# Kernel tuning notes

Measured on AMD Instinct MI355X. Metric: run time of the kernel, lower is better.

The kernel has to match this reference:

```python
import jax, jax.numpy as jnp
import numpy as np

N_NODES = 50000
N_EDGES = 800000
D_IN = 128
D_OUT = 128


def _seg_mean(values, seg_ids, num_segments):
    # values: [E, D] gathered messages; seg_ids: [E] destination ids
    s = jax.ops.segment_sum(values, seg_ids, num_segments=num_segments)
    deg = jax.ops.segment_sum(jnp.ones((values.shape[0],), values.dtype), seg_ids,
                              num_segments=num_segments)
    # DGL mean aggregation yields 0 for zero in-degree nodes
    return jnp.where(deg[:, None] > 0, s / jnp.maximum(deg, 1.0)[:, None], 0.0)


def setup_inputs() -> dict:
    key = jax.random.key(0)
    k1, k2, k3, k4, k5 = jax.random.split(key, 5)
    feat = jax.random.normal(k1, (N_NODES, D_IN), dtype=jnp.float32)
    src = jax.random.randint(k2, (N_EDGES,), 0, N_NODES, dtype=jnp.int32)
    dst = jax.random.randint(k3, (N_EDGES,), 0, N_NODES, dtype=jnp.int32)
    W = jax.random.normal(k4, (D_OUT, 3 * D_IN), dtype=jnp.float32) * (1.0 / np.sqrt(3 * D_IN))
    b = jax.random.normal(k5, (D_OUT,), dtype=jnp.float32) * 0.01
    return {"feat": feat, "src": src, "dst": dst, "W": W, "b": b}


def reference(feat, src, dst, W, b):
    n = feat.shape[0]
    # forward direction: message from src -> dst, mean over in-neighbors
    fwd_neigh = _seg_mean(feat[src], dst, n)          # [N, D]
    # backward direction: graph.reverse() swaps src/dst
    bwd_neigh = _seg_mean(feat[dst], src, n)          # [N, D]
    h = jnp.concatenate((feat, fwd_neigh, bwd_neigh), axis=1)  # [N, 3D]
    return h @ W.T + b
```

## Files before the change

kernel.cpp:

```cpp
#include <hip/hip_runtime.h>

#define DIM 128
#define CAP 64
#define CHUNK 2048

typedef __attribute__((ext_vector_type(8))) short bf16x8;
typedef __attribute__((ext_vector_type(4))) float f32x4;
typedef __attribute__((ext_vector_type(2))) float f32x2;

__device__ __forceinline__ unsigned short f2b(float f) {
  unsigned int u = __float_as_uint(f);
  return (unsigned short)((u + 0x7FFFu + ((u >> 16) & 1u)) >> 16);
}
__device__ __forceinline__ float blo(unsigned int v) { return __uint_as_float(v << 16); }
__device__ __forceinline__ float bhi(unsigned int v) { return __uint_as_float(v & 0xFFFF0000u); }

__global__ void k_prep(const float* __restrict__ feat, const float* __restrict__ W,
                       unsigned short* __restrict__ featb, unsigned short* __restrict__ Wb,
                       int N) {
  int i = blockIdx.x * blockDim.x + threadIdx.x;
  int ftotal = N * (DIM / 4);
  if (i < ftotal) {
    float4 v = ((const float4*)feat)[i];
    ushort4 o; o.x = f2b(v.x); o.y = f2b(v.y); o.z = f2b(v.z); o.w = f2b(v.w);
    ((ushort4*)featb)[i] = o;
  }
  const int wtotal = DIM * 3 * DIM / 4;
  if (i < wtotal) {
    float4 v = ((const float4*)W)[i];
    ushort4 o; o.x = f2b(v.x); o.y = f2b(v.y); o.z = f2b(v.z); o.w = f2b(v.w);
    ((ushort4*)Wb)[i] = o;
  }
}

__global__ __launch_bounds__(256) void k_gemmT(
    const unsigned short* __restrict__ featb, const unsigned short* __restrict__ Wb,
    const float* __restrict__ bias, unsigned short* __restrict__ g1b,
    unsigned char* __restrict__ g2f8, unsigned char* __restrict__ g3f8, int N) {
  const int wave = threadIdx.x >> 6, lane = threadIdx.x & 63;
  const int lr = lane & 15, lk = lane >> 4;
  const int nc = blockIdx.y;
  const int W0 = blockIdx.x * 4 + wave;
  const int TW = gridDim.x * 4;

  bf16x8 bf[4][4];
  #pragma unroll
  for (int kc = 0; kc < 4; ++kc)
    #pragma unroll
    for (int nf = 0; nf < 4; ++nf) {
      int n = nc * 64 + nf * 16 + lr;
      bf[kc][nf] = *(const bf16x8*)(Wb + (size_t)(n & 127) * 384 + (n >> 7) * 128
                                       + kc * 32 + lk * 8);
    }
  float bv[4];
  if (nc < 2) {
    #pragma unroll
    for (int nf = 0; nf < 4; ++nf) bv[nf] = bias[nc * 64 + nf * 16 + lr];
  }

  const int T = N >> 4;
  for (int t = W0; t < T; t += TW) {
    const int m0 = t * 16;
    bf16x8 a[4];
    #pragma unroll
    for (int kc = 0; kc < 4; ++kc)
      a[kc] = *(const bf16x8*)(featb + (size_t)(m0 + lr) * DIM + kc * 32 + lk * 8);
    f32x4 acc[4];
    #pragma unroll
    for (int nf = 0; nf < 4; ++nf) acc[nf] = (f32x4){0.f, 0.f, 0.f, 0.f};
    #pragma unroll
    for (int kc = 0; kc < 4; ++kc)
      #pragma unroll
      for (int nf = 0; nf < 4; ++nf)
        acc[nf] = __builtin_amdgcn_mfma_f32_16x16x32_bf16(a[kc], bf[kc][nf], acc[nf], 0, 0, 0);
    if (nc < 2) {
      #pragma unroll
      for (int nf = 0; nf < 4; ++nf)
        #pragma unroll
        for (int j = 0; j < 4; ++j)
          g1b[(size_t)(m0 + lk * 4 + j) * DIM + nc * 64 + nf * 16 + lr] =
              f2b(acc[nf][j] + bv[nf]);
    } else {
      unsigned char* gp = (nc < 4) ? g2f8 : g3f8;
      const int c0 = (nc & 1) * 64;
      #pragma unroll
      for (int nf = 0; nf < 4; ++nf)
        #pragma unroll
        for (int j = 0; j < 4; ++j) {
          unsigned int p8 = __builtin_amdgcn_cvt_pk_fp8_f32(acc[nf][j], acc[nf][j], 0, 0);
          gp[(size_t)(m0 + lk * 4 + j) * DIM + c0 + nf * 16 + lr] = (unsigned char)p8;
        }
    }
  }
}

__global__ __launch_bounds__(256) void k_bin(const int* __restrict__ src,
                                             const int* __restrict__ dst,
                                             unsigned int* __restrict__ scrF,
                                             unsigned int* __restrict__ scrB,
                                             int* __restrict__ offsF,
                                             int* __restrict__ offsB, int E) {
  __shared__ int fc[256], bc[256], fo[256], bo[256], sa[256], sb2[256];
  __shared__ unsigned int linf[CHUNK], linb[CHUNK];
  const int t = threadIdx.x;
  const int base = blockIdx.x * CHUNK;
  const int n = min(CHUNK, E - base);
  fc[t] = 0; bc[t] = 0;
  __syncthreads();
  int fbk[8], fsl[8], bsl[8], bbk[8];
  unsigned int fvv[8], bvv[8];
  #pragma unroll
  for (int j = 0; j < 8; ++j) {
    int e = base + j * 256 + t;
    fbk[j] = -1;
    if (e < E) {
      int s = src[e], d = dst[e];
      fbk[j] = d >> 8; fvv[j] = ((unsigned int)(d & 255) << 16) | (unsigned int)s;
      bbk[j] = s >> 8; bvv[j] = ((unsigned int)(s & 255) << 16) | (unsigned int)d;
      fsl[j] = atomicAdd(&fc[fbk[j]], 1);
      bsl[j] = atomicAdd(&bc[bbk[j]], 1);
    }
  }
  __syncthreads();
  sa[t] = fc[t]; sb2[t] = bc[t];
  __syncthreads();
  #pragma unroll
  for (int s = 1; s < 256; s <<= 1) {
    int va = sa[t] + ((t >= s) ? sa[t - s] : 0);
    int vb = sb2[t] + ((t >= s) ? sb2[t - s] : 0);
    __syncthreads();
    sa[t] = va; sb2[t] = vb;
    __syncthreads();
  }
  fo[t] = sa[t] - fc[t];
  bo[t] = sb2[t] - bc[t];
  __syncthreads();
  #pragma unroll
  for (int j = 0; j < 8; ++j) {
    if (fbk[j] >= 0) {
      linf[fo[fbk[j]] + fsl[j]] = fvv[j];
      linb[bo[bbk[j]] + bsl[j]] = bvv[j];
    }
  }
  offsF[blockIdx.x * 256 + t] = fo[t];
  offsB[blockIdx.x * 256 + t] = bo[t];
  __syncthreads();
  for (int k = t; k < n; k += 256) {
    scrF[base + k] = linf[k];
    scrB[base + k] = linb[k];
  }
}

__global__ __launch_bounds__(512) void k_csr(const unsigned int* __restrict__ scrF,
                                             const unsigned int* __restrict__ scrB,
                                             const int* __restrict__ offsF,
                                             const int* __restrict__ offsB,
                                             unsigned short* __restrict__ fnbr,
                                             unsigned short* __restrict__ bnbr,
                                             int* __restrict__ degF, int* __restrict__ degB,
                                             int N, int E, int nblk) {
  __shared__ int ncnt[256];
  __shared__ unsigned short nbuf[256][CAP];
  const int b = blockIdx.x;
  const int dir = blockIdx.y;
  const unsigned int* scr = dir ? scrB : scrF;
  const int* offs = dir ? offsB : offsF;
  const int t = threadIdx.x;
  if (t < 256) ncnt[t] = 0;
  __syncthreads();
  for (int i = t; i < nblk; i += 512) {
    int o = offs[i * 256 + b];
    int n = min(CHUNK, E - i * CHUNK);
    int nxt = (b < 255) ? offs[i * 256 + b + 1] : n;
    int cb = i * CHUNK;
    for (int k = o; k < nxt; ++k) {
      unsigned int v = scr[cb + k];
      int node8 = v >> 16;
      int slot = atomicAdd(&ncnt[node8], 1);
      if (slot < CAP) nbuf[node8][slot] = (unsigned short)(v & 0xFFFFu);
    }
  }
  __syncthreads();
  const int node0 = b * 256;
  const int nvalid = min(256, N - node0);
  if (nvalid <= 0) return;
  unsigned short* outp = (dir ? bnbr : fnbr) + (size_t)node0 * CAP;
  for (int idx = t; idx < nvalid * CAP; idx += 512)
    outp[idx] = nbuf[idx >> 6][idx & 63];
  int* deg = dir ? degB : degF;
  for (int u = t; u < nvalid; u += 512) deg[node0 + u] = ncnt[u];
}

__global__ void k_aggregate(const unsigned char* __restrict__ g2f8,
                            const unsigned char* __restrict__ g3f8,
                            const unsigned short* __restrict__ g1b,
                            const int* __restrict__ degF, const int* __restrict__ degB,
                            const unsigned short* __restrict__ fnbr,
                            const unsigned short* __restrict__ bnbr,
                            float* __restrict__ out, int N) {
  int node = blockIdx.x * (blockDim.x >> 6) + (threadIdx.x >> 6);
  if (node >= N) return;
  const int lane = threadIdx.x & 63;
  const int qg = lane >> 4;
  const int sub = lane & 15;

  const int degf = degF[node], degb = degB[node];
  const int capf = min(degf, CAP), capb = min(degb, CAP);
  const int fid = fnbr[(size_t)node * CAP + lane];
  const int bid = bnbr[(size_t)node * CAP + lane];

  const uint2* gf = (const uint2*)g2f8;
  const uint2* gb = (const uint2*)g3f8;
  float fa0=0,fa1=0,fa2=0,fa3=0,fa4=0,fa5=0,fa6=0,fa7=0;
  float ba0=0,ba1=0,ba2=0,ba3=0,ba4=0,ba5=0,ba6=0,ba7=0;
  const int gmax = (max(capf, capb) + 3) >> 2;
  #pragma unroll 4
  for (int g = 0; g < gmax; ++g) {
    int k = 4 * g + qg;
    int rf = __shfl(fid, k);
    int rb = __shfl(bid, k);
    if (k < capf) {
      uint2 v = gf[(size_t)rf * 16 + sub];
      f32x2 p0 = __builtin_amdgcn_cvt_pk_f32_fp8(v.x, 0);
      f32x2 p1 = __builtin_amdgcn_cvt_pk_f32_fp8(v.x, 1);
      f32x2 p2 = __builtin_amdgcn_cvt_pk_f32_fp8(v.y, 0);
      f32x2 p3 = __builtin_amdgcn_cvt_pk_f32_fp8(v.y, 1);
      fa0 += p0[0]; fa1 += p0[1]; fa2 += p1[0]; fa3 += p1[1];
      fa4 += p2[0]; fa5 += p2[1]; fa6 += p3[0]; fa7 += p3[1];
    }
    if (k < capb) {
      uint2 v = gb[(size_t)rb * 16 + sub];
      f32x2 p0 = __builtin_amdgcn_cvt_pk_f32_fp8(v.x, 0);
      f32x2 p1 = __builtin_amdgcn_cvt_pk_f32_fp8(v.x, 1);
      f32x2 p2 = __builtin_amdgcn_cvt_pk_f32_fp8(v.y, 0);
      f32x2 p3 = __builtin_amdgcn_cvt_pk_f32_fp8(v.y, 1);
      ba0 += p0[0]; ba1 += p0[1]; ba2 += p1[0]; ba3 += p1[1];
      ba4 += p2[0]; ba5 += p2[1]; ba6 += p3[0]; ba7 += p3[1];
    }
  }
  fa0 += __shfl_xor(fa0, 16); fa0 += __shfl_xor(fa0, 32);
  fa1 += __shfl_xor(fa1, 16); fa1 += __shfl_xor(fa1, 32);
  fa2 += __shfl_xor(fa2, 16); fa2 += __shfl_xor(fa2, 32);
  fa3 += __shfl_xor(fa3, 16); fa3 += __shfl_xor(fa3, 32);
  fa4 += __shfl_xor(fa4, 16); fa4 += __shfl_xor(fa4, 32);
  fa5 += __shfl_xor(fa5, 16); fa5 += __shfl_xor(fa5, 32);
  fa6 += __shfl_xor(fa6, 16); fa6 += __shfl_xor(fa6, 32);
  fa7 += __shfl_xor(fa7, 16); fa7 += __shfl_xor(fa7, 32);
  ba0 += __shfl_xor(ba0, 16); ba0 += __shfl_xor(ba0, 32);
  ba1 += __shfl_xor(ba1, 16); ba1 += __shfl_xor(ba1, 32);
  ba2 += __shfl_xor(ba2, 16); ba2 += __shfl_xor(ba2, 32);
  ba3 += __shfl_xor(ba3, 16); ba3 += __shfl_xor(ba3, 32);
  ba4 += __shfl_xor(ba4, 16); ba4 += __shfl_xor(ba4, 32);
  ba5 += __shfl_xor(ba5, 16); ba5 += __shfl_xor(ba5, 32);
  ba6 += __shfl_xor(ba6, 16); ba6 += __shfl_xor(ba6, 32);
  ba7 += __shfl_xor(ba7, 16); ba7 += __shfl_xor(ba7, 32);

  if (lane < 16) {
    const float sf = (degf > 0) ? 1.0f / (float)degf : 0.0f;
    const float sb = (degb > 0) ? 1.0f / (float)degb : 0.0f;
    uint4 g1v = ((const uint4*)g1b)[(size_t)node * 16 + lane];
    float4 u, v;
    u.x = blo(g1v.x) + fa0 * sf + ba0 * sb;
    u.y = bhi(g1v.x) + fa1 * sf + ba1 * sb;
    u.z = blo(g1v.y) + fa2 * sf + ba2 * sb;
    u.w = bhi(g1v.y) + fa3 * sf + ba3 * sb;
    v.x = blo(g1v.z) + fa4 * sf + ba4 * sb;
    v.y = bhi(g1v.z) + fa5 * sf + ba5 * sb;
    v.z = blo(g1v.w) + fa6 * sf + ba6 * sb;
    v.w = bhi(g1v.w) + fa7 * sf + ba7 * sb;
    float* op = out + (size_t)node * DIM + lane * 8;
    *(float4*)op = u; *(float4*)(op + 4) = v;
  }
}

extern "C" void kernel_launch(void* const* d_in, const int* in_sizes, int n_in,
                              void* d_out, int out_size, void* d_ws, size_t ws_size,
                              hipStream_t stream) {
  (void)n_in; (void)out_size; (void)ws_size;
  const float* feat = (const float*)d_in[0];
  const int*   src  = (const int*)d_in[1];
  const int*   dst  = (const int*)d_in[2];
  const float* W    = (const float*)d_in[3];
  const float* bias = (const float*)d_in[4];
  float* out = (float*)d_out;
  const int N = in_sizes[0] / DIM;
  const int E = in_sizes[1];
  const int nblk = (E + CHUNK - 1) / CHUNK;
  const int nbkt = (N + 255) / 256;

  char* ws = (char*)d_ws;
  size_t off = 0;
  auto take = [&](size_t bytes) -> void* {
    off = (off + 255) & ~(size_t)255;
    void* p = ws + off;
    off += bytes;
    return p;
  };
  unsigned int* scrF = (unsigned int*)take((size_t)nblk * CHUNK * 4);
  unsigned int* scrB = (unsigned int*)take((size_t)nblk * CHUNK * 4);
  int* offsF = (int*)take((size_t)nblk * 256 * 4);
  int* offsB = (int*)take((size_t)nblk * 256 * 4);
  unsigned short* fnbr = (unsigned short*)take((size_t)N * CAP * 2);
  unsigned short* bnbr = (unsigned short*)take((size_t)N * CAP * 2);
  int* degF = (int*)take((size_t)N * 4);
  int* degB = (int*)take((size_t)N * 4);
  unsigned short* featb = (unsigned short*)take((size_t)N * DIM * 2);
  unsigned short* Wb    = (unsigned short*)take((size_t)DIM * 3 * DIM * 2);
  unsigned short* g1b   = (unsigned short*)take((size_t)N * DIM * 2);
  unsigned char*  g2f8  = (unsigned char*)take((size_t)N * DIM);
  unsigned char*  g3f8  = (unsigned char*)take((size_t)N * DIM);

  int prep_threads = N * 32;
  k_prep<<<(prep_threads + 255) / 256, 256, 0, stream>>>(feat, W, featb, Wb, N);
  k_gemmT<<<dim3(128, 6), 256, 0, stream>>>(featb, Wb, bias, g1b, g2f8, g3f8, N);
  k_bin<<<nblk, 256, 0, stream>>>(src, dst, scrF, scrB, offsF, offsB, E);
  k_csr<<<dim3(nbkt, 2), 512, 0, stream>>>(scrF, scrB, offsF, offsB,
                                           fnbr, bnbr, degF, degB, N, E, nblk);
  k_aggregate<<<(N + 3) / 4, 256, 0, stream>>>(g2f8, g3f8, g1b, degF, degB,
                                               fnbr, bnbr, out, N);
}
```

Before: 104.0 us.

## Fuse prep with binning and CSR build with aggregation, prefetch GEMM A tiles

Merges the bf16 conversion kernel with the edge binning kernel into one launch, selected by block index, and fuses the CSR bucket build with the neighbor aggregation so neighbor lists and degrees stay in shared memory instead of going through global memory. The GEMM loop now loads the next A tile before computing the current one. The fused CSR/aggregate kernel runs only about 196 blocks of 512 threads, each aggregating 256 nodes, so much less parallelism is available for the gather-heavy aggregation phase, and it uses about 64KB of shared memory per block.

```diff
diff --git a/kernel.cpp b/kernel.cpp
--- a/kernel.cpp
+++ b/kernel.cpp
@@ -15,21 +15,78 @@
 __device__ __forceinline__ float blo(unsigned int v) { return __uint_as_float(v << 16); }
 __device__ __forceinline__ float bhi(unsigned int v) { return __uint_as_float(v & 0xFFFF0000u); }
 
-__global__ void k_prep(const float* __restrict__ feat, const float* __restrict__ W,
-                       unsigned short* __restrict__ featb, unsigned short* __restrict__ Wb,
-                       int N) {
-  int i = blockIdx.x * blockDim.x + threadIdx.x;
-  int ftotal = N * (DIM / 4);
-  if (i < ftotal) {
-    float4 v = ((const float4*)feat)[i];
-    ushort4 o; o.x = f2b(v.x); o.y = f2b(v.y); o.z = f2b(v.z); o.w = f2b(v.w);
-    ((ushort4*)featb)[i] = o;
-  }
-  const int wtotal = DIM * 3 * DIM / 4;
-  if (i < wtotal) {
-    float4 v = ((const float4*)W)[i];
-    ushort4 o; o.x = f2b(v.x); o.y = f2b(v.y); o.z = f2b(v.z); o.w = f2b(v.w);
-    ((ushort4*)Wb)[i] = o;
+__global__ __launch_bounds__(256) void k_prepbin(
+    const float* __restrict__ feat, const float* __restrict__ W,
+    const int* __restrict__ src, const int* __restrict__ dst,
+    unsigned short* __restrict__ featb, unsigned short* __restrict__ Wb,
+    unsigned int* __restrict__ scrF, unsigned int* __restrict__ scrB,
+    int* __restrict__ offsF, int* __restrict__ offsB, int N, int E, int nblk) {
+  __shared__ int fc[256], bc[256], fo[256], bo[256], sa[256], sb2[256];
+  __shared__ unsigned int linf[CHUNK], linb[CHUNK];
+  const int t = threadIdx.x;
+
+  if (blockIdx.x >= nblk) {
+    int i = (blockIdx.x - nblk) * 256 + t;
+    int ftotal = N * (DIM / 4);
+    if (i < ftotal) {
+      float4 v = ((const float4*)feat)[i];
+      ushort4 o; o.x = f2b(v.x); o.y = f2b(v.y); o.z = f2b(v.z); o.w = f2b(v.w);
+      ((ushort4*)featb)[i] = o;
+    }
+    const int wtotal = DIM * 3 * DIM / 4;
+    if (i < wtotal) {
+      float4 v = ((const float4*)W)[i];
+      ushort4 o; o.x = f2b(v.x); o.y = f2b(v.y); o.z = f2b(v.z); o.w = f2b(v.w);
+      ((ushort4*)Wb)[i] = o;
+    }
+    return;
+  }
+
+  const int base = blockIdx.x * CHUNK;
+  const int n = min(CHUNK, E - base);
+  fc[t] = 0; bc[t] = 0;
+  __syncthreads();
+  int fbk[8], fsl[8], bsl[8], bbk[8];
+  unsigned int fvv[8], bvv[8];
+  #pragma unroll
+  for (int j = 0; j < 8; ++j) {
+    int e = base + j * 256 + t;
+    fbk[j] = -1;
+    if (e < E) {
+      int s = src[e], d = dst[e];
+      fbk[j] = d >> 8; fvv[j] = ((unsigned int)(d & 255) << 16) | (unsigned int)s;
+      bbk[j] = s >> 8; bvv[j] = ((unsigned int)(s & 255) << 16) | (unsigned int)d;
+      fsl[j] = atomicAdd(&fc[fbk[j]], 1);
+      bsl[j] = atomicAdd(&bc[bbk[j]], 1);
+    }
+  }
+  __syncthreads();
+  sa[t] = fc[t]; sb2[t] = bc[t];
+  __syncthreads();
+  #pragma unroll
+  for (int s = 1; s < 256; s <<= 1) {
+    int va = sa[t] + ((t >= s) ? sa[t - s] : 0);
+    int vb = sb2[t] + ((t >= s) ? sb2[t - s] : 0);
+    __syncthreads();
+    sa[t] = va; sb2[t] = vb;
+    __syncthreads();
+  }
+  fo[t] = sa[t] - fc[t];
+  bo[t] = sb2[t] - bc[t];
+  __syncthreads();
+  #pragma unroll
+  for (int j = 0; j < 8; ++j) {
+    if (fbk[j] >= 0) {
+      linf[fo[fbk[j]] + fsl[j]] = fvv[j];
+      linb[bo[bbk[j]] + bsl[j]] = bvv[j];
+    }
+  }
+  offsF[blockIdx.x * 256 + t] = fo[t];
+  offsB[blockIdx.x * 256 + t] = bo[t];
+  __syncthreads();
+  for (int k = t; k < n; k += 256) {
+    scrF[base + k] = linf[k];
+    scrB[base + k] = linb[k];
   }
 }
 
@@ -59,12 +116,22 @@
   }
 
   const int T = N >> 4;
-  for (int t = W0; t < T; t += TW) {
+  int t = W0;
+  bf16x8 a[4];
+  if (t < T) {
+    #pragma unroll
+    for (int kc = 0; kc < 4; ++kc)
+      a[kc] = *(const bf16x8*)(featb + (size_t)(t * 16 + lr) * DIM + kc * 32 + lk * 8);
+  }
+  while (t < T) {
+    const int tn = t + TW;
+    bf16x8 an[4];
+    if (tn < T) {
+      #pragma unroll
+      for (int kc = 0; kc < 4; ++kc)
+        an[kc] = *(const bf16x8*)(featb + (size_t)(tn * 16 + lr) * DIM + kc * 32 + lk * 8);
+    }
     const int m0 = t * 16;
-    bf16x8 a[4];
-    #pragma unroll
-    for (int kc = 0; kc < 4; ++kc)
-      a[kc] = *(const bf16x8*)(featb + (size_t)(m0 + lr) * DIM + kc * 32 + lk * 8);
     f32x4 acc[4];
     #pragma unroll
     for (int nf = 0; nf < 4; ++nf) acc[nf] = (f32x4){0.f, 0.f, 0.f, 0.f};
@@ -91,185 +158,118 @@
           gp[(size_t)(m0 + lk * 4 + j) * DIM + c0 + nf * 16 + lr] = (unsigned char)p8;
         }
     }
-  }
-}
-
-__global__ __launch_bounds__(256) void k_bin(const int* __restrict__ src,
-                                             const int* __restrict__ dst,
-                                             unsigned int* __restrict__ scrF,
-                                             unsigned int* __restrict__ scrB,
-                                             int* __restrict__ offsF,
-                                             int* __restrict__ offsB, int E) {
-  __shared__ int fc[256], bc[256], fo[256], bo[256], sa[256], sb2[256];
-  __shared__ unsigned int linf[CHUNK], linb[CHUNK];
+    #pragma unroll
+    for (int kc = 0; kc < 4; ++kc) a[kc] = an[kc];
+    t = tn;
+  }
+}
+
+__global__ __launch_bounds__(512) void k_csragg(
+    const unsigned int* __restrict__ scrF, const unsigned int* __restrict__ scrB,
+    const int* __restrict__ offsF, const int* __restrict__ offsB,
+    const unsigned char* __restrict__ g2f8, const unsigned char* __restrict__ g3f8,
+    const unsigned short* __restrict__ g1b, float* __restrict__ out,
+    int N, int E, int nblk) {
+  __shared__ int ncF[256], ncB[256];
+  __shared__ unsigned short nbF[256][CAP], nbB[256][CAP];
+  const int b = blockIdx.x;
   const int t = threadIdx.x;
-  const int base = blockIdx.x * CHUNK;
-  const int n = min(CHUNK, E - base);
-  fc[t] = 0; bc[t] = 0;
-  __syncthreads();
-  int fbk[8], fsl[8], bsl[8], bbk[8];
-  unsigned int fvv[8], bvv[8];
-  #pragma unroll
-  for (int j = 0; j < 8; ++j) {
-    int e = base + j * 256 + t;
-    fbk[j] = -1;
-    if (e < E) {
-      int s = src[e], d = dst[e];
-      fbk[j] = d >> 8; fvv[j] = ((unsigned int)(d & 255) << 16) | (unsigned int)s;
-      bbk[j] = s >> 8; bvv[j] = ((unsigned int)(s & 255) << 16) | (unsigned int)d;
-      fsl[j] = atomicAdd(&fc[fbk[j]], 1);
-      bsl[j] = atomicAdd(&bc[bbk[j]], 1);
-    }
-  }
-  __syncthreads();
-  sa[t] = fc[t]; sb2[t] = bc[t];
-  __syncthreads();
-  #pragma unroll
-  for (int s = 1; s < 256; s <<= 1) {
-    int va = sa[t] + ((t >= s) ? sa[t - s] : 0);
-    int vb = sb2[t] + ((t >= s) ? sb2[t - s] : 0);
-    __syncthreads();
-    sa[t] = va; sb2[t] = vb;
-    __syncthreads();
-  }
-  fo[t] = sa[t] - fc[t];
-  bo[t] = sb2[t] - bc[t];
-  __syncthreads();
-  #pragma unroll
-  for (int j = 0; j < 8; ++j) {
-    if (fbk[j] >= 0) {
-      linf[fo[fbk[j]] + fsl[j]] = fvv[j];
-      linb[bo[bbk[j]] + bsl[j]] = bvv[j];
-    }
-  }
-  offsF[blockIdx.x * 256 + t] = fo[t];
-  offsB[blockIdx.x * 256 + t] = bo[t];
-  __syncthreads();
-  for (int k = t; k < n; k += 256) {
-    scrF[base + k] = linf[k];
-    scrB[base + k] = linb[k];
-  }
-}
-
-__global__ __launch_bounds__(512) void k_csr(const unsigned int* __restrict__ scrF,
-                                             const unsigned int* __restrict__ scrB,
-                                             const int* __restrict__ offsF,
-                                             const int* __restrict__ offsB,
-                                             unsigned short* __restrict__ fnbr,
-                                             unsigned short* __restrict__ bnbr,
-                                             int* __restrict__ degF, int* __restrict__ degB,
-                                             int N, int E, int nblk) {
-  __shared__ int ncnt[256];
-  __shared__ unsigned short nbuf[256][CAP];
-  const int b = blockIdx.x;
-  const int dir = blockIdx.y;
-  const unsigned int* scr = dir ? scrB : scrF;
-  const int* offs = dir ? offsB : offsF;
-  const int t = threadIdx.x;
-  if (t < 256) ncnt[t] = 0;
+  if (t < 256) { ncF[t] = 0; ncB[t] = 0; }
   __syncthreads();
   for (int i = t; i < nblk; i += 512) {
-    int o = offs[i * 256 + b];
-    int n = min(CHUNK, E - i * CHUNK);
-    int nxt = (b < 255) ? offs[i * 256 + b + 1] : n;
-    int cb = i * CHUNK;
-    for (int k = o; k < nxt; ++k) {
-      unsigned int v = scr[cb + k];
-      int node8 = v >> 16;
-      int slot = atomicAdd(&ncnt[node8], 1);
-      if (slot < CAP) nbuf[node8][slot] = (unsigned short)(v & 0xFFFFu);
-    }
-  }
-  __syncthreads();
-  const int node0 = b * 256;
-  const int nvalid = min(256, N - node0);
-  if (nvalid <= 0) return;
-  unsigned short* outp = (dir ? bnbr : fnbr) + (size_t)node0 * CAP;
-  for (int idx = t; idx < nvalid * CAP; idx += 512)
-    outp[idx] = nbuf[idx >> 6][idx & 63];
-  int* deg = dir ? degB : degF;
-  for (int u = t; u < nvalid; u += 512) deg[node0 + u] = ncnt[u];
-}
-
-__global__ void k_aggregate(const unsigned char* __restrict__ g2f8,
-                            const unsigned char* __restrict__ g3f8,
-                            const unsigned short* __restrict__ g1b,
-                            const int* __restrict__ degF, const int* __restrict__ degB,
-                            const unsigned short* __restrict__ fnbr,
-                            const unsigned short* __restrict__ bnbr,
-                            float* __restrict__ out, int N) {
-  int node = blockIdx.x * (blockDim.x >> 6) + (threadIdx.x >> 6);
-  if (node >= N) return;
-  const int lane = threadIdx.x & 63;
+    const int cb = i * CHUNK;
+    const int n = min(CHUNK, E - cb);
+    int o = offsF[i * 256 + b];
+    int nx = (b < 255) ? offsF[i * 256 + b + 1] : n;
+    for (int k = o; k < nx; ++k) {
+      unsigned int v = scrF[cb + k];
+      int n8 = v >> 16;
+      int sl = atomicAdd(&ncF[n8], 1);
+      if (sl < CAP) nbF[n8][sl] = (unsigned short)(v & 0xFFFFu);
+    }
+    o = offsB[i * 256 + b];
+    nx = (b < 255) ? offsB[i * 256 + b + 1] : n;
+    for (int k = o; k < nx; ++k) {
+      unsigned int v = scrB[cb + k];
+      int n8 = v >> 16;
+      int sl = atomicAdd(&ncB[n8], 1);
+      if (sl < CAP) nbB[n8][sl] = (unsigned short)(v & 0xFFFFu);
+    }
+  }
+  __syncthreads();
+
+  const int wv = t >> 6, lane = t & 63;
   const int qg = lane >> 4;
   const int sub = lane & 15;
-
-  const int degf = degF[node], degb = degB[node];
-  const int capf = min(degf, CAP), capb = min(degb, CAP);
-  const int fid = fnbr[(size_t)node * CAP + lane];
-  const int bid = bnbr[(size_t)node * CAP + lane];
-
   const uint2* gf = (const uint2*)g2f8;
   const uint2* gb = (const uint2*)g3f8;
-  float fa0=0,fa1=0,fa2=0,fa3=0,fa4=0,fa5=0,fa6=0,fa7=0;
-  float ba0=0,ba1=0,ba2=0,ba3=0,ba4=0,ba5=0,ba6=0,ba7=0;
-  const int gmax = (max(capf, capb) + 3) >> 2;
-  #pragma unroll 4
-  for (int g = 0; g < gmax; ++g) {
-    int k = 4 * g + qg;
-    int rf = __shfl(fid, k);
-    int rb = __shfl(bid, k);
-    if (k < capf) {
-      uint2 v = gf[(size_t)rf * 16 + sub];
-      f32x2 p0 = __builtin_amdgcn_cvt_pk_f32_fp8(v.x, 0);
-      f32x2 p1 = __builtin_amdgcn_cvt_pk_f32_fp8(v.x, 1);
-      f32x2 p2 = __builtin_amdgcn_cvt_pk_f32_fp8(v.y, 0);
-      f32x2 p3 = __builtin_amdgcn_cvt_pk_f32_fp8(v.y, 1);
-      fa0 += p0[0]; fa1 += p0[1]; fa2 += p1[0]; fa3 += p1[1];
-      fa4 += p2[0]; fa5 += p2[1]; fa6 += p3[0]; fa7 += p3[1];
-    }
-    if (k < capb) {
-      uint2 v = gb[(size_t)rb * 16 + sub];
-      f32x2 p0 = __builtin_amdgcn_cvt_pk_f32_fp8(v.x, 0);
-      f32x2 p1 = __builtin_amdgcn_cvt_pk_f32_fp8(v.x, 1);
-      f32x2 p2 = __builtin_amdgcn_cvt_pk_f32_fp8(v.y, 0);
-      f32x2 p3 = __builtin_amdgcn_cvt_pk_f32_fp8(v.y, 1);
-      ba0 += p0[0]; ba1 += p0[1]; ba2 += p1[0]; ba3 += p1[1];
-      ba4 += p2[0]; ba5 += p2[1]; ba6 += p3[0]; ba7 += p3[1];
-    }
-  }
-  fa0 += __shfl_xor(fa0, 16); fa0 += __shfl_xor(fa0, 32);
-  fa1 += __shfl_xor(fa1, 16); fa1 += __shfl_xor(fa1, 32);
-  fa2 += __shfl_xor(fa2, 16); fa2 += __shfl_xor(fa2, 32);
-  fa3 += __shfl_xor(fa3, 16); fa3 += __shfl_xor(fa3, 32);
-  fa4 += __shfl_xor(fa4, 16); fa4 += __shfl_xor(fa4, 32);
-  fa5 += __shfl_xor(fa5, 16); fa5 += __shfl_xor(fa5, 32);
-  fa6 += __shfl_xor(fa6, 16); fa6 += __shfl_xor(fa6, 32);
-  fa7 += __shfl_xor(fa7, 16); fa7 += __shfl_xor(fa7, 32);
-  ba0 += __shfl_xor(ba0, 16); ba0 += __shfl_xor(ba0, 32);
-  ba1 += __shfl_xor(ba1, 16); ba1 += __shfl_xor(ba1, 32);
-  ba2 += __shfl_xor(ba2, 16); ba2 += __shfl_xor(ba2, 32);
-  ba3 += __shfl_xor(ba3, 16); ba3 += __shfl_xor(ba3, 32);
-  ba4 += __shfl_xor(ba4, 16); ba4 += __shfl_xor(ba4, 32);
-  ba5 += __shfl_xor(ba5, 16); ba5 += __shfl_xor(ba5, 32);
-  ba6 += __shfl_xor(ba6, 16); ba6 += __shfl_xor(ba6, 32);
-  ba7 += __shfl_xor(ba7, 16); ba7 += __shfl_xor(ba7, 32);
-
-  if (lane < 16) {
-    const float sf = (degf > 0) ? 1.0f / (float)degf : 0.0f;
-    const float sb = (degb > 0) ? 1.0f / (float)degb : 0.0f;
-    uint4 g1v = ((const uint4*)g1b)[(size_t)node * 16 + lane];
-    float4 u, v;
-    u.x = blo(g1v.x) + fa0 * sf + ba0 * sb;
-    u.y = bhi(g1v.x) + fa1 * sf + ba1 * sb;
-    u.z = blo(g1v.y) + fa2 * sf + ba2 * sb;
-    u.w = bhi(g1v.y) + fa3 * sf + ba3 * sb;
-    v.x = blo(g1v.z) + fa4 * sf + ba4 * sb;
-    v.y = bhi(g1v.z) + fa5 * sf + ba5 * sb;
-    v.z = blo(g1v.w) + fa6 * sf + ba6 * sb;
-    v.w = bhi(g1v.w) + fa7 * sf + ba7 * sb;
-    float* op = out + (size_t)node * DIM + lane * 8;
-    *(float4*)op = u; *(float4*)(op + 4) = v;
+
+  for (int j = 0; j < 32; ++j) {
+    const int n8 = wv * 32 + j;
+    const int node = b * 256 + n8;
+    if (node >= N) break;
+    const int degf = ncF[n8], degb = ncB[n8];
+    const int capf = min(degf, CAP), capb = min(degb, CAP);
+    f32x2 f01 = {0.f, 0.f}, f23 = {0.f, 0.f}, f45 = {0.f, 0.f}, f67 = {0.f, 0.f};
+    f32x2 b01 = {0.f, 0.f}, b23 = {0.f, 0.f}, b45 = {0.f, 0.f}, b67 = {0.f, 0.f};
+    const int gmax = (max(capf, capb) + 3) >> 2;
+    #pragma unroll 4
+    for (int g = 0; g < gmax; ++g) {
+      int k = 4 * g + qg;
+      if (k < capf) {
+        int rf = nbF[n8][k];
+        uint2 v = gf[(size_t)rf * 16 + sub];
+        f01 += __builtin_amdgcn_cvt_pk_f32_fp8(v.x, 0);
+        f23 += __builtin_amdgcn_cvt_pk_f32_fp8(v.x, 1);
+        f45 += __builtin_amdgcn_cvt_pk_f32_fp8(v.y, 0);
+        f67 += __builtin_amdgcn_cvt_pk_f32_fp8(v.y, 1);
+      }
+      if (k < capb) {
+        int rb = nbB[n8][k];
+        uint2 v = gb[(size_t)rb * 16 + sub];
+        b01 += __builtin_amdgcn_cvt_pk_f32_fp8(v.x, 0);
+        b23 += __builtin_amdgcn_cvt_pk_f32_fp8(v.x, 1);
+        b45 += __builtin_amdgcn_cvt_pk_f32_fp8(v.y, 0);
+        b67 += __builtin_amdgcn_cvt_pk_f32_fp8(v.y, 1);
+      }
+    }
+    float fa0 = f01[0], fa1 = f01[1], fa2 = f23[0], fa3 = f23[1];
+    float fa4 = f45[0], fa5 = f45[1], fa6 = f67[0], fa7 = f67[1];
+    float ba0 = b01[0], ba1 = b01[1], ba2 = b23[0], ba3 = b23[1];
+    float ba4 = b45[0], ba5 = b45[1], ba6 = b67[0], ba7 = b67[1];
+    fa0 += __shfl_xor(fa0, 16); fa0 += __shfl_xor(fa0, 32);
+    fa1 += __shfl_xor(fa1, 16); fa1 += __shfl_xor(fa1, 32);
+    fa2 += __shfl_xor(fa2, 16); fa2 += __shfl_xor(fa2, 32);
+    fa3 += __shfl_xor(fa3, 16); fa3 += __shfl_xor(fa3, 32);
+    fa4 += __shfl_xor(fa4, 16); fa4 += __shfl_xor(fa4, 32);
+    fa5 += __shfl_xor(fa5, 16); fa5 += __shfl_xor(fa5, 32);
+    fa6 += __shfl_xor(fa6, 16); fa6 += __shfl_xor(fa6, 32);
+    fa7 += __shfl_xor(fa7, 16); fa7 += __shfl_xor(fa7, 32);
+    ba0 += __shfl_xor(ba0, 16); ba0 += __shfl_xor(ba0, 32);
+    ba1 += __shfl_xor(ba1, 16); ba1 += __shfl_xor(ba1, 32);
+    ba2 += __shfl_xor(ba2, 16); ba2 += __shfl_xor(ba2, 32);
+    ba3 += __shfl_xor(ba3, 16); ba3 += __shfl_xor(ba3, 32);
+    ba4 += __shfl_xor(ba4, 16); ba4 += __shfl_xor(ba4, 32);
+    ba5 += __shfl_xor(ba5, 16); ba5 += __shfl_xor(ba5, 32);
+    ba6 += __shfl_xor(ba6, 16); ba6 += __shfl_xor(ba6, 32);
+    ba7 += __shfl_xor(ba7, 16); ba7 += __shfl_xor(ba7, 32);
+
+    if (lane < 16) {
+      const float sf = (degf > 0) ? 1.0f / (float)degf : 0.0f;
+      const float sb = (degb > 0) ? 1.0f / (float)degb : 0.0f;
+      uint4 g1v = ((const uint4*)g1b)[(size_t)node * 16 + lane];
+      float4 u, v;
+      u.x = blo(g1v.x) + fa0 * sf + ba0 * sb;
+      u.y = bhi(g1v.x) + fa1 * sf + ba1 * sb;
+      u.z = blo(g1v.y) + fa2 * sf + ba2 * sb;
+      u.w = bhi(g1v.y) + fa3 * sf + ba3 * sb;
+      v.x = blo(g1v.z) + fa4 * sf + ba4 * sb;
+      v.y = bhi(g1v.z) + fa5 * sf + ba5 * sb;
+      v.z = blo(g1v.w) + fa6 * sf + ba6 * sb;
+      v.w = bhi(g1v.w) + fa7 * sf + ba7 * sb;
+      float* op = out + (size_t)node * DIM + lane * 8;
+      *(float4*)op = u; *(float4*)(op + 4) = v;
+    }
   }
 }
 
@@ -300,22 +300,16 @@
   unsigned int* scrB = (unsigned int*)take((size_t)nblk * CHUNK * 4);
   int* offsF = (int*)take((size_t)nblk * 256 * 4);
   int* offsB = (int*)take((size_t)nblk * 256 * 4);
-  unsigned short* fnbr = (unsigned short*)take((size_t)N * CAP * 2);
-  unsigned short* bnbr = (unsigned short*)take((size_t)N * CAP * 2);
-  int* degF = (int*)take((size_t)N * 4);
-  int* degB = (int*)take((size_t)N * 4);
   unsigned short* featb = (unsigned short*)take((size_t)N * DIM * 2);
   unsigned short* Wb    = (unsigned short*)take((size_t)DIM * 3 * DIM * 2);
   unsigned short* g1b   = (unsigned short*)take((size_t)N * DIM * 2);
   unsigned char*  g2f8  = (unsigned char*)take((size_t)N * DIM);
   unsigned char*  g3f8  = (unsigned char*)take((size_t)N * DIM);
 
-  int prep_threads = N * 32;
-  k_prep<<<(prep_threads + 255) / 256, 256, 0, stream>>>(feat, W, featb, Wb, N);
+  const int prep_blocks = (N * 32 + 255) / 256;
+  k_prepbin<<<nblk + prep_blocks, 256, 0, stream>>>(
+      feat, W, src, dst, featb, Wb, scrF, scrB, offsF, offsB, N, E, nblk);
   k_gemmT<<<dim3(128, 6), 256, 0, stream>>>(featb, Wb, bias, g1b, g2f8, g3f8, N);
-  k_bin<<<nblk, 256, 0, stream>>>(src, dst, scrF, scrB, offsF, offsB, E);
-  k_csr<<<dim3(nbkt, 2), 512, 0, stream>>>(scrF, scrB, offsF, offsB,
-                                           fnbr, bnbr, degF, degB, N, E, nblk);
-  k_aggregate<<<(N + 3) / 4, 256, 0, stream>>>(g2f8, g3f8, g1b, degF, degB,
-                                               fnbr, bnbr, out, N);
-}
+  k_csragg<<<nbkt, 512, 0, stream>>>(scrF, scrB, offsF, offsB,
+                                     g2f8, g3f8, g1b, out, N, E, nblk);
+}
```

Measured after the change: 190.4 us. 1.83x slower.

## Merge independent kernels into combined launches, prefetch GEMM tiles, pack fp8 accumulation

Applied to the files above, without the earlier changes.

The prep and bin kernels are merged into one launch, with blocks partitioned by index. The CSR-build and GEMM kernels are merged the same way, so independent work runs concurrently and launch gaps shrink from five kernels to three. The GEMM loop now software-prefetches the next A tile, using 512-thread blocks with 8 waves. The aggregate loop accumulates into packed f32x2 vectors with a deeper unroll. The merged kernels carry the larger LDS footprint onto all blocks, which may reduce occupancy for the prep and GEMM blocks.

```diff
diff --git a/kernel.cpp b/kernel.cpp
--- a/kernel.cpp
+++ b/kernel.cpp
@@ -15,33 +15,131 @@
 __device__ __forceinline__ float blo(unsigned int v) { return __uint_as_float(v << 16); }
 __device__ __forceinline__ float bhi(unsigned int v) { return __uint_as_float(v & 0xFFFF0000u); }
 
-__global__ void k_prep(const float* __restrict__ feat, const float* __restrict__ W,
-                       unsigned short* __restrict__ featb, unsigned short* __restrict__ Wb,
-                       int N) {
-  int i = blockIdx.x * blockDim.x + threadIdx.x;
-  int ftotal = N * (DIM / 4);
-  if (i < ftotal) {
-    float4 v = ((const float4*)feat)[i];
-    ushort4 o; o.x = f2b(v.x); o.y = f2b(v.y); o.z = f2b(v.z); o.w = f2b(v.w);
-    ((ushort4*)featb)[i] = o;
-  }
-  const int wtotal = DIM * 3 * DIM / 4;
-  if (i < wtotal) {
-    float4 v = ((const float4*)W)[i];
-    ushort4 o; o.x = f2b(v.x); o.y = f2b(v.y); o.z = f2b(v.z); o.w = f2b(v.w);
-    ((ushort4*)Wb)[i] = o;
-  }
-}
-
-__global__ __launch_bounds__(256) void k_gemmT(
+__global__ __launch_bounds__(256) void k_prepbin(
+    const float* __restrict__ feat, const float* __restrict__ W,
+    const int* __restrict__ src, const int* __restrict__ dst,
+    unsigned short* __restrict__ featb, unsigned short* __restrict__ Wb,
+    unsigned int* __restrict__ scrF, unsigned int* __restrict__ scrB,
+    int* __restrict__ offsF, int* __restrict__ offsB, int N, int E, int nblk) {
+  __shared__ int fc[256], bc[256], fo[256], bo[256], sa[256], sb2[256];
+  __shared__ unsigned int linf[CHUNK], linb[CHUNK];
+  const int t = threadIdx.x;
+
+  if (blockIdx.x >= nblk) {
+    int i = (blockIdx.x - nblk) * 256 + t;
+    int ftotal = N * (DIM / 4);
+    if (i < ftotal) {
+      float4 v = ((const float4*)feat)[i];
+      ushort4 o; o.x = f2b(v.x); o.y = f2b(v.y); o.z = f2b(v.z); o.w = f2b(v.w);
+      ((ushort4*)featb)[i] = o;
+    }
+    const int wtotal = DIM * 3 * DIM / 4;
+    if (i < wtotal) {
+      float4 v = ((const float4*)W)[i];
+      ushort4 o; o.x = f2b(v.x); o.y = f2b(v.y); o.z = f2b(v.z); o.w = f2b(v.w);
+      ((ushort4*)Wb)[i] = o;
+    }
+    return;
+  }
+
+  const int base = blockIdx.x * CHUNK;
+  const int n = min(CHUNK, E - base);
+  fc[t] = 0; bc[t] = 0;
+  __syncthreads();
+  int fbk[8], fsl[8], bsl[8], bbk[8];
+  unsigned int fvv[8], bvv[8];
+  #pragma unroll
+  for (int j = 0; j < 8; ++j) {
+    int e = base + j * 256 + t;
+    fbk[j] = -1;
+    if (e < E) {
+      int s = src[e], d = dst[e];
+      fbk[j] = d >> 8; fvv[j] = ((unsigned int)(d & 255) << 16) | (unsigned int)s;
+      bbk[j] = s >> 8; bvv[j] = ((unsigned int)(s & 255) << 16) | (unsigned int)d;
+      fsl[j] = atomicAdd(&fc[fbk[j]], 1);
+      bsl[j] = atomicAdd(&bc[bbk[j]], 1);
+    }
+  }
+  __syncthreads();
+  sa[t] = fc[t]; sb2[t] = bc[t];
+  __syncthreads();
+  #pragma unroll
+  for (int s = 1; s < 256; s <<= 1) {
+    int va = sa[t] + ((t >= s) ? sa[t - s] : 0);
+    int vb = sb2[t] + ((t >= s) ? sb2[t - s] : 0);
+    __syncthreads();
+    sa[t] = va; sb2[t] = vb;
+    __syncthreads();
+  }
+  fo[t] = sa[t] - fc[t];
+  bo[t] = sb2[t] - bc[t];
+  __syncthreads();
+  #pragma unroll
+  for (int j = 0; j < 8; ++j) {
+    if (fbk[j] >= 0) {
+      linf[fo[fbk[j]] + fsl[j]] = fvv[j];
+      linb[bo[bbk[j]] + bsl[j]] = bvv[j];
+    }
+  }
+  offsF[blockIdx.x * 256 + t] = fo[t];
+  offsB[blockIdx.x * 256 + t] = bo[t];
+  __syncthreads();
+  for (int k = t; k < n; k += 256) {
+    scrF[base + k] = linf[k];
+    scrB[base + k] = linb[k];
+  }
+}
+
+__global__ __launch_bounds__(512) void k_gemmcsr(
     const unsigned short* __restrict__ featb, const unsigned short* __restrict__ Wb,
     const float* __restrict__ bias, unsigned short* __restrict__ g1b,
-    unsigned char* __restrict__ g2f8, unsigned char* __restrict__ g3f8, int N) {
-  const int wave = threadIdx.x >> 6, lane = threadIdx.x & 63;
+    unsigned char* __restrict__ g2f8, unsigned char* __restrict__ g3f8,
+    const unsigned int* __restrict__ scrF, const unsigned int* __restrict__ scrB,
+    const int* __restrict__ offsF, const int* __restrict__ offsB,
+    unsigned short* __restrict__ fnbr, unsigned short* __restrict__ bnbr,
+    int* __restrict__ degF, int* __restrict__ degB,
+    int N, int E, int nblk, int nbkt) {
+  __shared__ int ncnt[256];
+  __shared__ unsigned short nbuf[256][CAP];
+  const int t = threadIdx.x;
+
+  if (blockIdx.x < (unsigned)(2 * nbkt)) {
+    const int b = blockIdx.x >> 1;
+    const int dir = blockIdx.x & 1;
+    const unsigned int* scr = dir ? scrB : scrF;
+    const int* offs = dir ? offsB : offsF;
+    if (t < 256) ncnt[t] = 0;
+    __syncthreads();
+    for (int i = t; i < nblk; i += 512) {
+      int o = offs[i * 256 + b];
+      int n = min(CHUNK, E - i * CHUNK);
+      int nxt = (b < 255) ? offs[i * 256 + b + 1] : n;
+      int cb = i * CHUNK;
+      for (int k = o; k < nxt; ++k) {
+        unsigned int v = scr[cb + k];
+        int node8 = v >> 16;
+        int slot = atomicAdd(&ncnt[node8], 1);
+        if (slot < CAP) nbuf[node8][slot] = (unsigned short)(v & 0xFFFFu);
+      }
+    }
+    __syncthreads();
+    const int node0 = b * 256;
+    const int nvalid = min(256, N - node0);
+    if (nvalid <= 0) return;
+    unsigned short* outp = (dir ? bnbr : fnbr) + (size_t)node0 * CAP;
+    for (int idx = t; idx < nvalid * CAP; idx += 512)
+      outp[idx] = nbuf[idx >> 6][idx & 63];
+    int* deg = dir ? degB : degF;
+    for (int u = t; u < nvalid; u += 512) deg[node0 + u] = ncnt[u];
+    return;
+  }
+
+  const int gid = blockIdx.x - 2 * nbkt;
+  const int wave = t >> 6, lane = t & 63;
   const int lr = lane & 15, lk = lane >> 4;
-  const int nc = blockIdx.y;
-  const int W0 = blockIdx.x * 4 + wave;
-  const int TW = gridDim.x * 4;
+  const int nc = gid >> 6;
+  const int W0 = (gid & 63) * 8 + wave;
+  const int TW = 64 * 8;
 
   bf16x8 bf[4][4];
   #pragma unroll
@@ -59,12 +157,22 @@
   }
 
   const int T = N >> 4;
-  for (int t = W0; t < T; t += TW) {
-    const int m0 = t * 16;
-    bf16x8 a[4];
+  int tt = W0;
+  bf16x8 a[4];
+  if (tt < T) {
     #pragma unroll
     for (int kc = 0; kc < 4; ++kc)
-      a[kc] = *(const bf16x8*)(featb + (size_t)(m0 + lr) * DIM + kc * 32 + lk * 8);
+      a[kc] = *(const bf16x8*)(featb + (size_t)(tt * 16 + lr) * DIM + kc * 32 + lk * 8);
+  }
+  while (tt < T) {
+    const int tn = tt + TW;
+    bf16x8 an[4];
+    if (tn < T) {
+      #pragma unroll
+      for (int kc = 0; kc < 4; ++kc)
+        an[kc] = *(const bf16x8*)(featb + (size_t)(tn * 16 + lr) * DIM + kc * 32 + lk * 8);
+    }
+    const int m0 = tt * 16;
     f32x4 acc[4];
     #pragma unroll
     for (int nf = 0; nf < 4; ++nf) acc[nf] = (f32x4){0.f, 0.f, 0.f, 0.f};
@@ -91,104 +199,10 @@
           gp[(size_t)(m0 + lk * 4 + j) * DIM + c0 + nf * 16 + lr] = (unsigned char)p8;
         }
     }
-  }
-}
-
-__global__ __launch_bounds__(256) void k_bin(const int* __restrict__ src,
-                                             const int* __restrict__ dst,
-                                             unsigned int* __restrict__ scrF,
-                                             unsigned int* __restrict__ scrB,
-                                             int* __restrict__ offsF,
-                                             int* __restrict__ offsB, int E) {
-  __shared__ int fc[256], bc[256], fo[256], bo[256], sa[256], sb2[256];
-  __shared__ unsigned int linf[CHUNK], linb[CHUNK];
-  const int t = threadIdx.x;
-  const int base = blockIdx.x * CHUNK;
-  const int n = min(CHUNK, E - base);
-  fc[t] = 0; bc[t] = 0;
-  __syncthreads();
-  int fbk[8], fsl[8], bsl[8], bbk[8];
-  unsigned int fvv[8], bvv[8];
-  #pragma unroll
-  for (int j = 0; j < 8; ++j) {
-    int e = base + j * 256 + t;
-    fbk[j] = -1;
-    if (e < E) {
-      int s = src[e], d = dst[e];
-      fbk[j] = d >> 8; fvv[j] = ((unsigned int)(d & 255) << 16) | (unsigned int)s;
-      bbk[j] = s >> 8; bvv[j] = ((unsigned int)(s & 255) << 16) | (unsigned int)d;
-      fsl[j] = atomicAdd(&fc[fbk[j]], 1);
-      bsl[j] = atomicAdd(&bc[bbk[j]], 1);
-    }
-  }
-  __syncthreads();
-  sa[t] = fc[t]; sb2[t] = bc[t];
-  __syncthreads();
-  #pragma unroll
-  for (int s = 1; s < 256; s <<= 1) {
-    int va = sa[t] + ((t >= s) ? sa[t - s] : 0);
-    int vb = sb2[t] + ((t >= s) ? sb2[t - s] : 0);
-    __syncthreads();
-    sa[t] = va; sb2[t] = vb;
-    __syncthreads();
-  }
-  fo[t] = sa[t] - fc[t];
-  bo[t] = sb2[t] - bc[t];
-  __syncthreads();
-  #pragma unroll
-  for (int j = 0; j < 8; ++j) {
-    if (fbk[j] >= 0) {
-      linf[fo[fbk[j]] + fsl[j]] = fvv[j];
-      linb[bo[bbk[j]] + bsl[j]] = bvv[j];
-    }
-  }
-  offsF[blockIdx.x * 256 + t] = fo[t];
-  offsB[blockIdx.x * 256 + t] = bo[t];
-  __syncthreads();
-  for (int k = t; k < n; k += 256) {
-    scrF[base + k] = linf[k];
-    scrB[base + k] = linb[k];
-  }
-}
-
-__global__ __launch_bounds__(512) void k_csr(const unsigned int* __restrict__ scrF,
-                                             const unsigned int* __restrict__ scrB,
-                                             const int* __restrict__ offsF,
-                                             const int* __restrict__ offsB,
-                                             unsigned short* __restrict__ fnbr,
-                                             unsigned short* __restrict__ bnbr,
-                                             int* __restrict__ degF, int* __restrict__ degB,
-                                             int N, int E, int nblk) {
-  __shared__ int ncnt[256];
-  __shared__ unsigned short nbuf[256][CAP];
-  const int b = blockIdx.x;
-  const int dir = blockIdx.y;
-  const unsigned int* scr = dir ? scrB : scrF;
-  const int* offs = dir ? offsB : offsF;
-  const int t = threadIdx.x;
-  if (t < 256) ncnt[t] = 0;
-  __syncthreads();
-  for (int i = t; i < nblk; i += 512) {
-    int o = offs[i * 256 + b];
-    int n = min(CHUNK, E - i * CHUNK);
-    int nxt = (b < 255) ? offs[i * 256 + b + 1] : n;
-    int cb = i * CHUNK;
-    for (int k = o; k < nxt; ++k) {
-      unsigned int v = scr[cb + k];
-      int node8 = v >> 16;
-      int slot = atomicAdd(&ncnt[node8], 1);
-      if (slot < CAP) nbuf[node8][slot] = (unsigned short)(v & 0xFFFFu);
-    }
-  }
-  __syncthreads();
-  const int node0 = b * 256;
-  const int nvalid = min(256, N - node0);
-  if (nvalid <= 0) return;
-  unsigned short* outp = (dir ? bnbr : fnbr) + (size_t)node0 * CAP;
-  for (int idx = t; idx < nvalid * CAP; idx += 512)
-    outp[idx] = nbuf[idx >> 6][idx & 63];
-  int* deg = dir ? degB : degF;
-  for (int u = t; u < nvalid; u += 512) deg[node0 + u] = ncnt[u];
+    #pragma unroll
+    for (int kc = 0; kc < 4; ++kc) a[kc] = an[kc];
+    tt = tn;
+  }
 }
 
 __global__ void k_aggregate(const unsigned char* __restrict__ g2f8,
@@ -211,33 +225,33 @@
 
   const uint2* gf = (const uint2*)g2f8;
   const uint2* gb = (const uint2*)g3f8;
-  float fa0=0,fa1=0,fa2=0,fa3=0,fa4=0,fa5=0,fa6=0,fa7=0;
-  float ba0=0,ba1=0,ba2=0,ba3=0,ba4=0,ba5=0,ba6=0,ba7=0;
+  f32x2 f01 = {0.f, 0.f}, f23 = {0.f, 0.f}, f45 = {0.f, 0.f}, f67 = {0.f, 0.f};
+  f32x2 b01 = {0.f, 0.f}, b23 = {0.f, 0.f}, b45 = {0.f, 0.f}, b67 = {0.f, 0.f};
   const int gmax = (max(capf, capb) + 3) >> 2;
-  #pragma unroll 4
+  #pragma unroll 8
   for (int g = 0; g < gmax; ++g) {
     int k = 4 * g + qg;
     int rf = __shfl(fid, k);
     int rb = __shfl(bid, k);
     if (k < capf) {
       uint2 v = gf[(size_t)rf * 16 + sub];
-      f32x2 p0 = __builtin_amdgcn_cvt_pk_f32_fp8(v.x, 0);
-      f32x2 p1 = __builtin_amdgcn_cvt_pk_f32_fp8(v.x, 1);
-      f32x2 p2 = __builtin_amdgcn_cvt_pk_f32_fp8(v.y, 0);
-      f32x2 p3 = __builtin_amdgcn_cvt_pk_f32_fp8(v.y, 1);
-      fa0 += p0[0]; fa1 += p0[1]; fa2 += p1[0]; fa3 += p1[1];
-      fa4 += p2[0]; fa5 += p2[1]; fa6 += p3[0]; fa7 += p3[1];
+      f01 += __builtin_amdgcn_cvt_pk_f32_fp8(v.x, 0);
+      f23 += __builtin_amdgcn_cvt_pk_f32_fp8(v.x, 1);
+      f45 += __builtin_amdgcn_cvt_pk_f32_fp8(v.y, 0);
+      f67 += __builtin_amdgcn_cvt_pk_f32_fp8(v.y, 1);
     }
     if (k < capb) {
       uint2 v = gb[(size_t)rb * 16 + sub];
-      f32x2 p0 = __builtin_amdgcn_cvt_pk_f32_fp8(v.x, 0);
-      f32x2 p1 = __builtin_amdgcn_cvt_pk_f32_fp8(v.x, 1);
-      f32x2 p2 = __builtin_amdgcn_cvt_pk_f32_fp8(v.y, 0);
-      f32x2 p3 = __builtin_amdgcn_cvt_pk_f32_fp8(v.y, 1);
-      ba0 += p0[0]; ba1 += p0[1]; ba2 += p1[0]; ba3 += p1[1];
-      ba4 += p2[0]; ba5 += p2[1]; ba6 += p3[0]; ba7 += p3[1];
-    }
-  }
+      b01 += __builtin_amdgcn_cvt_pk_f32_fp8(v.x, 0);
+      b23 += __builtin_amdgcn_cvt_pk_f32_fp8(v.x, 1);
+      b45 += __builtin_amdgcn_cvt_pk_f32_fp8(v.y, 0);
+      b67 += __builtin_amdgcn_cvt_pk_f32_fp8(v.y, 1);
+    }
+  }
+  float fa0 = f01[0], fa1 = f01[1], fa2 = f23[0], fa3 = f23[1];
+  float fa4 = f45[0], fa5 = f45[1], fa6 = f67[0], fa7 = f67[1];
+  float ba0 = b01[0], ba1 = b01[1], ba2 = b23[0], ba3 = b23[1];
+  float ba4 = b45[0], ba5 = b45[1], ba6 = b67[0], ba7 = b67[1];
   fa0 += __shfl_xor(fa0, 16); fa0 += __shfl_xor(fa0, 32);
   fa1 += __shfl_xor(fa1, 16); fa1 += __shfl_xor(fa1, 32);
   fa2 += __shfl_xor(fa2, 16); fa2 += __shfl_xor(fa2, 32);
@@ -310,12 +324,12 @@
   unsigned char*  g2f8  = (unsigned char*)take((size_t)N * DIM);
   unsigned char*  g3f8  = (unsigned char*)take((size_t)N * DIM);
 
-  int prep_threads = N * 32;
-  k_prep<<<(prep_threads + 255) / 256, 256, 0, stream>>>(feat, W, featb, Wb, N);
-  k_gemmT<<<dim3(128, 6), 256, 0, stream>>>(featb, Wb, bias, g1b, g2f8, g3f8, N);
-  k_bin<<<nblk, 256, 0, stream>>>(src, dst, scrF, scrB, offsF, offsB, E);
-  k_csr<<<dim3(nbkt, 2), 512, 0, stream>>>(scrF, scrB, offsF, offsB,
-                                           fnbr, bnbr, degF, degB, N, E, nblk);
+  const int prep_blocks = (N * 32 + 255) / 256;
+  k_prepbin<<<nblk + prep_blocks, 256, 0, stream>>>(
+      feat, W, src, dst, featb, Wb, scrF, scrB, offsF, offsB, N, E, nblk);
+  k_gemmcsr<<<2 * nbkt + 384, 512, 0, stream>>>(
+      featb, Wb, bias, g1b, g2f8, g3f8, scrF, scrB, offsF, offsB,
+      fnbr, bnbr, degF, degB, N, E, nblk, nbkt);
   k_aggregate<<<(N + 3) / 4, 256, 0, stream>>>(g2f8, g3f8, g1b, degF, degB,
                                                fnbr, bnbr, out, N);
 }
```

Result: faster. 101.2 us (-2.6%).
